# Performance work log

Measured on AMD Instinct MI355X. Metric: run time of the kernel, lower is better.

Reference implementation:

```python
import jax, jax.numpy as jnp
import numpy as np

N_NODES = 10000
N_EDGES = 160000
N_GRAPHS = 100
D = 32
E_DIM = 6
Q = 96
C = 2
EPS = 1e-5
S2S_STEPS = 3


def _bn(x, gamma, beta):
    # BatchNorm1d in training mode: normalize over the batch (row) axis
    mu = jnp.mean(x, axis=0)
    var = jnp.var(x, axis=0)
    return gamma * (x - mu) * jax.lax.rsqrt(var + EPS) + beta


def _mlp_layer(x, w, b, gamma, beta):
    # Linear -> ReLU -> BatchNorm1d (one block of the MLP helper)
    return _bn(jax.nn.relu(x @ w.T + b), gamma, beta)


def _nnconv(x, src, dst, edge_attr, nw, nb, ng, nbeta, root, bias):
    # edge MLP -> per-edge [D, D] weight matrices
    w = _mlp_layer(edge_attr, nw, nb, ng, nbeta).reshape(-1, D, D)  # [E, D, D]
    msg = jnp.einsum('ei,eio->eo', x[src], w)                       # per-edge matvec
    agg = jax.ops.segment_sum(msg, dst, num_segments=N_NODES)      # aggr='add'
    return agg + x @ root + bias                                    # root weight + bias


def _set2set(x, batch, w_ih, w_hh, b_ih, b_hh):
    h = jnp.zeros((N_GRAPHS, Q), x.dtype)
    c = jnp.zeros((N_GRAPHS, Q), x.dtype)
    q_star = jnp.zeros((N_GRAPHS, 2 * Q), x.dtype)
    for _ in range(S2S_STEPS):
        gates = q_star @ w_ih.T + b_ih + h @ w_hh.T + b_hh  # [B, 4Q], gate order i,f,g,o
        i, f, g, o = jnp.split(gates, 4, axis=1)
        c = jax.nn.sigmoid(f) * c + jax.nn.sigmoid(i) * jnp.tanh(g)
        h = jax.nn.sigmoid(o) * jnp.tanh(c)
        e = jnp.sum(x * h[batch], axis=-1)  # [N] attention logits
        emax = jax.ops.segment_max(e, batch, num_segments=N_GRAPHS)
        emax = jnp.where(jnp.isfinite(emax), emax, 0.0)
        a = jnp.exp(e - emax[batch])
        asum = jax.ops.segment_sum(a, batch, num_segments=N_GRAPHS)
        a = a / asum[batch]
        r = jax.ops.segment_sum(a[:, None] * x, batch, num_segments=N_GRAPHS)  # [B, Q]
        q_star = jnp.concatenate([h, r], axis=1)
    return q_star  # [B, 2Q]


def setup_inputs() -> dict:
    key = jax.random.key(0)
    ks = iter(jax.random.split(key, 48))
    def rn(shape, fan_in):
        return jax.random.normal(next(ks), shape, dtype=jnp.float32) * (1.0 / np.sqrt(fan_in))
    d = {}
    d['x'] = jax.random.normal(next(ks), (N_NODES, D), dtype=jnp.float32)
    d['edge_attr'] = jax.random.uniform(next(ks), (N_EDGES, E_DIM), dtype=jnp.float32)
    # conv1 edge-MLP + root + bias
    d['c1_nn_w'] = rn((D * D, E_DIM), E_DIM); d['c1_nn_b'] = jnp.zeros((D * D,), jnp.float32)
    d['c1_nn_g'] = jnp.ones((D * D,), jnp.float32); d['c1_nn_beta'] = jnp.zeros((D * D,), jnp.float32)
    d['c1_root'] = rn((D, D), D); d['c1_bias'] = jnp.zeros((D,), jnp.float32)
    # conv2
    d['c2_nn_w'] = rn((D * D, E_DIM), E_DIM); d['c2_nn_b'] = jnp.zeros((D * D,), jnp.float32)
    d['c2_nn_g'] = jnp.ones((D * D,), jnp.float32); d['c2_nn_beta'] = jnp.zeros((D * D,), jnp.float32)
    d['c2_root'] = rn((D, D), D); d['c2_bias'] = jnp.zeros((D,), jnp.float32)
    # lin1: MLP([2D, Q])
    d['lin1_w'] = rn((Q, 2 * D), 2 * D); d['lin1_b'] = jnp.zeros((Q,), jnp.float32)
    d['lin1_g'] = jnp.ones((Q,), jnp.float32); d['lin1_beta'] = jnp.zeros((Q,), jnp.float32)
    # Set2Set LSTM: input 2Q -> hidden Q
    d['lstm_w_ih'] = rn((4 * Q, 2 * Q), 2 * Q); d['lstm_w_hh'] = rn((4 * Q, Q), Q)
    d['lstm_b_ih'] = jnp.zeros((4 * Q,), jnp.float32); d['lstm_b_hh'] = jnp.zeros((4 * Q,), jnp.float32)
    # S2Slin: Linear(2Q, Q)
    d['s2s_w'] = rn((Q, 2 * Q), 2 * Q); d['s2s_b'] = jnp.zeros((Q,), jnp.float32)
    # mlp1: MLP([Q, Q, C])
    d['m1_w'] = rn((Q, Q), Q); d['m1_b'] = jnp.zeros((Q,), jnp.float32)
    d['m1_g'] = jnp.ones((Q,), jnp.float32); d['m1_beta'] = jnp.zeros((Q,), jnp.float32)
    d['m2_w'] = rn((C, Q), Q); d['m2_b'] = jnp.zeros((C,), jnp.float32)
    d['m2_g'] = jnp.ones((C,), jnp.float32); d['m2_beta'] = jnp.zeros((C,), jnp.float32)
    # graph structure
    d['edge_src'] = jax.random.randint(next(ks), (N_EDGES,), 0, N_NODES, dtype=jnp.int32)
    d['edge_dst'] = jax.random.randint(next(ks), (N_EDGES,), 0, N_NODES, dtype=jnp.int32)
    d['batch'] = jnp.sort(jax.random.randint(next(ks), (N_NODES,), 0, N_GRAPHS, dtype=jnp.int32))
    return d


def reference(x, edge_attr,
              c1_nn_w, c1_nn_b, c1_nn_g, c1_nn_beta, c1_root, c1_bias,
              c2_nn_w, c2_nn_b, c2_nn_g, c2_nn_beta, c2_root, c2_bias,
              lin1_w, lin1_b, lin1_g, lin1_beta,
              lstm_w_ih, lstm_w_hh, lstm_b_ih, lstm_b_hh,
              s2s_w, s2s_b,
              m1_w, m1_b, m1_g, m1_beta,
              m2_w, m2_b, m2_g, m2_beta,
              edge_src, edge_dst, batch):
    x1 = _nnconv(x, edge_src, edge_dst, edge_attr, c1_nn_w, c1_nn_b, c1_nn_g, c1_nn_beta, c1_root, c1_bias)
    x2 = _nnconv(x1, edge_src, edge_dst, edge_attr, c2_nn_w, c2_nn_b, c2_nn_g, c2_nn_beta, c2_root, c2_bias)
    xc = _mlp_layer(jnp.concatenate([x1, x2], axis=1), lin1_w, lin1_b, lin1_g, lin1_beta)  # [N, Q]
    qs = _set2set(xc, batch, lstm_w_ih, lstm_w_hh, lstm_b_ih, lstm_b_hh)                   # [B, 2Q]
    xg = qs @ s2s_w.T + s2s_b                                                               # [B, Q]
    xg = _mlp_layer(xg, m1_w, m1_b, m1_g, m1_beta)
    out = _mlp_layer(xg, m2_w, m2_b, m2_g, m2_beta)                                         # [B, C]
    return out
```

## Files before the change

kernel.cpp:

```cpp
#include <hip/hip_runtime.h>
#include <math.h>

#define NN 10000
#define NE 160000
#define NG 100
#define DD 32
#define QQ 96
#define EPS 1e-5f
#define S2SCAP 128

typedef float f2 __attribute__((ext_vector_type(2)));

__global__ __launch_bounds__(512) void k_stats7(const float* __restrict__ ea,
        const float* __restrict__ w1, const float* __restrict__ b1,
        const float* __restrict__ w2, const float* __restrict__ b2,
        float* __restrict__ stats) {
    const int tid = threadIdx.x;
    const int chunk = blockIdx.x >> 1;
    const int ct = ((blockIdx.x & 1) << 9) | tid;
    const float* wr1 = w1 + ct * 6;
    const float* wr2 = w2 + ct * 6;
    f2 W0 = {wr1[0], wr2[0]}, W1 = {wr1[1], wr2[1]}, W2 = {wr1[2], wr2[2]};
    f2 W3 = {wr1[3], wr2[3]}, W4 = {wr1[4], wr2[4]}, W5 = {wr1[5], wr2[5]};
    f2 Bb = {b1[ct], b2[ct]};
    f2 S = {0.f, 0.f}, SS = {0.f, 0.f};
    const float* base = ea + chunk * 1536;
#pragma unroll 4
    for (int q = 0; q < 128; ++q) {
        float4 q0 = *reinterpret_cast<const float4*>(base + q * 12);
        float4 q1 = *reinterpret_cast<const float4*>(base + q * 12 + 4);
        float4 q2 = *reinterpret_cast<const float4*>(base + q * 12 + 8);
        {
            f2 y = Bb;
            y = q0.x * W0 + y; y = q0.y * W1 + y; y = q0.z * W2 + y;
            y = q0.w * W3 + y; y = q1.x * W4 + y; y = q1.y * W5 + y;
            f2 r = {fmaxf(y.x, 0.f), fmaxf(y.y, 0.f)};
            S = S + r; SS = r * r + SS;
        }
        {
            f2 y = Bb;
            y = q1.z * W0 + y; y = q1.w * W1 + y; y = q2.x * W2 + y;
            y = q2.y * W3 + y; y = q2.z * W4 + y; y = q2.w * W5 + y;
            f2 r = {fmaxf(y.x, 0.f), fmaxf(y.y, 0.f)};
            S = S + r; SS = r * r + SS;
        }
    }
    atomicAdd(&stats[ct], S.x);
    atomicAdd(&stats[1024 + ct], SS.x);
    atomicAdd(&stats[2048 + ct], S.y);
    atomicAdd(&stats[3072 + ct], SS.y);
}

__global__ __launch_bounds__(256) void k_root(const float* __restrict__ x,
        const float* __restrict__ root, const float* __restrict__ bias,
        float* __restrict__ out,
        int doFin, const float* __restrict__ stats,
        const float* __restrict__ g1, const float* __restrict__ beta1,
        const float* __restrict__ g2, const float* __restrict__ beta2,
        const float* __restrict__ nw1, const float* __restrict__ nb1,
        const float* __restrict__ nw2, const float* __restrict__ nb2,
        float* __restrict__ wpack) {
    const int tid = threadIdx.x;
    if (doFin && blockIdx.x == gridDim.x - 1) {
        const float invE = 1.f / NE;
        for (int j = tid; j < 2048; j += 256) {
            int cv = j >> 10, col = j & 1023;
            const float* st = stats + cv * 2048;
            const float* g = cv ? g2 : g1;
            const float* bt = cv ? beta2 : beta1;
            const float* w = (cv ? nw2 : nw1) + col * 6;
            const float* nb = cv ? nb2 : nb1;
            float mean = st[col] * invE;
            float var = fmaxf(st[1024 + col] * invE - mean * mean, 0.f);
            float a = g[col] * rsqrtf(var + EPS);
            float b = bt[col] - mean * a;
            float* rec = wpack + cv * 12288 + col * 12;
            rec[0] = w[0]; rec[1] = w[1]; rec[2] = w[2];
            rec[3] = w[3]; rec[4] = w[4]; rec[5] = w[5];
            rec[6] = nb[col]; rec[7] = a; rec[8] = b;
        }
        return;
    }
    __shared__ float rlds[1024];
#pragma unroll
    for (int r = 0; r < 4; ++r) rlds[tid + 256 * r] = root[tid + 256 * r];
    __syncthreads();
    const int o = tid & 31;
    const int gg = tid >> 5;
    const int n = blockIdx.x * 8 + gg;
    if (n >= NN) return;
    const int half = tid & 32;
    float xs = x[n * 32 + o];
    float acc = bias[o];
#pragma unroll
    for (int i = 0; i < 32; ++i) {
        float xi = __shfl(xs, half | i);
        acc = fmaf(xi, rlds[i * 32 + o], acc);
    }
    out[n * 32 + o] = acc;
}

#define CACCP(PTR, XK, M) { \
    float4 _wa = *reinterpret_cast<const float4*>(PTR); \
    float4 _wb = *reinterpret_cast<const float4*>((PTR) + 4); \
    float _bv = (PTR)[8]; \
    float _y = _wb.z; \
    _y = fmaf(e0, _wa.x, _y); _y = fmaf(e1, _wa.y, _y); _y = fmaf(e2, _wa.z, _y); \
    _y = fmaf(e3, _wa.w, _y); _y = fmaf(e4, _wb.x, _y); _y = fmaf(e5, _wb.y, _y); \
    float _t = fmaf(_wb.w, fmaxf(_y, 0.f), _bv); M = fmaf(XK, _t, M); }

__global__ __launch_bounds__(256) void k_conv(const float* __restrict__ xin,
        const float* __restrict__ ea, const int* __restrict__ src, const int* __restrict__ dst,
        const float* __restrict__ wp, float* __restrict__ agg) {
    __shared__ float part[4][16][32];
    const int tid = threadIdx.x;
    const int lane = tid & 63;
    const int w = tid >> 6;
    const int p = lane >> 5;
    const int o = lane & 31;

    const float* r0 = wp + (((((w << 3) + 0 + p) << 5) | o) * 12);
    const float* r1 = wp + (((((w << 3) + 2 + p) << 5) | o) * 12);
    const float* r2 = wp + (((((w << 3) + 4 + p) << 5) | o) * 12);
    const float* r3 = wp + (((((w << 3) + 6 + p) << 5) | o) * 12);

    const int base0 = blockIdx.x * 80;
#pragma unroll 1
    for (int ch = 0; ch < 5; ++ch) {
        const int base = base0 + ch * 16;
#pragma unroll 4
        for (int m = 0; m < 16; ++m) {
            const int e = base + m;
            const int sc = src[e];
            const float* er = ea + e * 6;
            float e0 = er[0], e1 = er[1], e2 = er[2], e3 = er[3], e4 = er[4], e5 = er[5];
            const float* xr = xin + sc * 32 + (w << 3);
            float4 qa = *reinterpret_cast<const float4*>(xr);
            float4 qb = *reinterpret_cast<const float4*>(xr + 4);
            float xA = p ? qa.y : qa.x, xB = p ? qa.w : qa.z;
            float xC = p ? qb.y : qb.x, xD = p ? qb.w : qb.z;
            float msg = 0.f;
            CACCP(r0, xA, msg) CACCP(r1, xB, msg) CACCP(r2, xC, msg) CACCP(r3, xD, msg)
            msg += __shfl_xor(msg, 32, 64);
            if (p == 0) part[w][m][o] = msg;
        }
        __syncthreads();
        {
            const int m = tid >> 5;
            const int e = base + m;
            const int dd = dst[e];
            float sum = part[0][m][o] + part[1][m][o] + part[2][m][o] + part[3][m][o];
            atomicAdd(&agg[dd * 32 + o], sum);
            const int m2 = m + 8;
            const int e2 = base + m2;
            const int dd2 = dst[e2];
            float sum2 = part[0][m2][o] + part[1][m2][o] + part[2][m2][o] + part[3][m2][o];
            atomicAdd(&agg[dd2 * 32 + o], sum2);
        }
        __syncthreads();
    }
}

__global__ __launch_bounds__(384) void k_lin1a(const float* __restrict__ x1,
        const float* __restrict__ x2, const float* __restrict__ lw, const float* __restrict__ lb,
        float* __restrict__ pre, float* __restrict__ gsum, float* __restrict__ gsumsq) {
    __shared__ float cat[4][64];
    __shared__ float sh_s[96], sh_ss[96];
    const int tid = threadIdx.x;
    const int np = tid / 96;
    const int q = tid - np * 96;
    float w[64];
#pragma unroll
    for (int k = 0; k < 64; ++k) w[k] = lw[q * 64 + k];
    const float bq = lb[q];
    float s = 0.f, ss = 0.f;
    for (int nb = blockIdx.x * 4; nb < NN; nb += gridDim.x * 4) {
        __syncthreads();
        if (tid < 256) {
            int n2 = tid >> 6, k = tid & 63;
            cat[n2][k] = (k < 32) ? x1[(nb + n2) * 32 + k] : x2[(nb + n2) * 32 + (k - 32)];
        }
        __syncthreads();
        float v = bq;
#pragma unroll
        for (int k = 0; k < 64; ++k) v = fmaf(cat[np][k], w[k], v);
        float r = fmaxf(v, 0.f);
        pre[(nb + np) * 96 + q] = r;
        s += r; ss = fmaf(r, r, ss);
    }
    __syncthreads();
    if (tid < 96) { sh_s[tid] = 0.f; sh_ss[tid] = 0.f; }
    __syncthreads();
    atomicAdd(&sh_s[q], s);
    atomicAdd(&sh_ss[q], ss);
    __syncthreads();
    if (tid < 96) {
        atomicAdd(&gsum[tid], sh_s[tid]);
        atomicAdd(&gsumsq[tid], sh_ss[tid]);
    }
}

__global__ __launch_bounds__(512) void k_s2s(const float* __restrict__ pre,
        const int* __restrict__ batch,
        const float* __restrict__ gsum, const float* __restrict__ gsumsq,
        const float* __restrict__ lg, const float* __restrict__ lbeta,
        const float* __restrict__ w_ih, const float* __restrict__ w_hh,
        const float* __restrict__ b_ih, const float* __restrict__ b_hh,
        float* __restrict__ qs_g, float* __restrict__ e_ws) {
    __shared__ float xcs[S2SCAP * 96];
    __shared__ float aws[S2SCAP];
    __shared__ float qs[192], h[96], c[96], gates[384];
    __shared__ float ab_a[96], ab_b[96], hA[96], bh[96];
    __shared__ float redm[8], reds[8];
    __shared__ float racc_s[5][96];
    __shared__ float sh_scal[3];
    __shared__ int sse[2];
    const int tid = threadIdx.x;
    const int wid = tid >> 6, lane = tid & 63;
    const int b = blockIdx.x;
    if (tid < 2) {
        int key = b + tid, lo = 0, hi = NN;
        while (lo < hi) { int mid = (lo + hi) >> 1; if (batch[mid] < key) lo = mid + 1; else hi = mid; }
        sse[tid] = lo;
    }
    if (tid < 192) qs[tid] = 0.f;
    if (tid < 96) {
        h[tid] = 0.f; c[tid] = 0.f;
        const float invN = 1.f / NN;
        float mean = gsum[tid] * invN;
        float var = fmaxf(gsumsq[tid] * invN - mean * mean, 0.f);
        float a = lg[tid] * rsqrtf(var + EPS);
        ab_a[tid] = a;
        ab_b[tid] = lbeta[tid] - mean * a;
    }
    __syncthreads();
    const int s = sse[0], t = sse[1];
    const int cnt = t - s;
    const bool fits = (cnt <= S2SCAP);
    if (fits) {
        for (int idx = tid; idx < cnt * 96; idx += 512) xcs[idx] = pre[s * 96 + idx];
    }
    const float* pb = fits ? (const float*)xcs : (pre + s * 96);
    float* ewp = fits ? (float*)aws : (e_ws + s);
    __syncthreads();
    for (int step = 0; step < 3; ++step) {
        if (tid < 384) {
            float acc = b_ih[tid] + b_hh[tid];
            const float* wi = &w_ih[tid * 192];
#pragma unroll 8
            for (int k = 0; k < 192; ++k) acc = fmaf(qs[k], wi[k], acc);
            const float* wh = &w_hh[tid * 96];
#pragma unroll 8
            for (int k = 0; k < 96; ++k) acc = fmaf(h[k], wh[k], acc);
            gates[tid] = acc;
        }
        __syncthreads();
        if (tid < 96) {
            float ig = 1.f / (1.f + __expf(-gates[tid]));
            float fg = 1.f / (1.f + __expf(-gates[96 + tid]));
            float gg = tanhf(gates[192 + tid]);
            float og = 1.f / (1.f + __expf(-gates[288 + tid]));
            float cn = fg * c[tid] + ig * gg;
            c[tid] = cn;
            float hn = og * tanhf(cn);
            h[tid] = hn;
            hA[tid] = ab_a[tid] * hn;
            bh[tid] = ab_b[tid] * hn;
        }
        __syncthreads();
        if (tid < 64) {
            float v = bh[tid] + (tid < 32 ? bh[64 + tid] : 0.f);
#pragma unroll
            for (int off = 32; off > 0; off >>= 1) v += __shfl_down(v, off);
            if (tid == 0) sh_scal[2] = v;
        }
        __syncthreads();
        const float hb = sh_scal[2];
        float pmax = -INFINITY;
        for (int u = tid; u < cnt; u += 512) {
            const float* xr = pb + u * 96;
            float acc = hb;
#pragma unroll
            for (int k4 = 0; k4 < 24; ++k4) {
                float4 v = *reinterpret_cast<const float4*>(xr + k4 * 4);
                acc = fmaf(v.x, hA[k4 * 4], acc);
                acc = fmaf(v.y, hA[k4 * 4 + 1], acc);
                acc = fmaf(v.z, hA[k4 * 4 + 2], acc);
                acc = fmaf(v.w, hA[k4 * 4 + 3], acc);
            }
            ewp[u] = acc;
            pmax = fmaxf(pmax, acc);
        }
#pragma unroll
        for (int off = 32; off > 0; off >>= 1) pmax = fmaxf(pmax, __shfl_down(pmax, off));
        if (lane == 0) redm[wid] = pmax;
        __syncthreads();
        if (tid == 0) {
            float m = redm[0];
#pragma unroll
            for (int i = 1; i < 8; ++i) m = fmaxf(m, redm[i]);
            if (!isfinite(m)) m = 0.f;
            sh_scal[0] = m;
        }
        __syncthreads();
        const float emax = sh_scal[0];
        float pa = 0.f;
        for (int u = tid; u < cnt; u += 512) {
            float a = __expf(ewp[u] - emax);
            ewp[u] = a;
            pa += a;
        }
#pragma unroll
        for (int off = 32; off > 0; off >>= 1) pa += __shfl_down(pa, off);
        if (lane == 0) reds[wid] = pa;
        __syncthreads();
        if (tid == 0) {
            float a2 = 0.f;
#pragma unroll
            for (int i = 0; i < 8; ++i) a2 += reds[i];
            sh_scal[1] = (a2 > 0.f) ? 1.f / a2 : 0.f;
        }
        __syncthreads();
        const int g = tid / 96, q = tid - g * 96;
        if (tid < 480) {
            float racc = 0.f;
            for (int u = g; u < cnt; u += 5)
                racc = fmaf(ewp[u], pb[u * 96 + q], racc);
            racc_s[g][q] = racc;
        }
        __syncthreads();
        if (tid < 96) {
            float inv = sh_scal[1];
            float racc5 = racc_s[0][tid] + racc_s[1][tid] + racc_s[2][tid]
                        + racc_s[3][tid] + racc_s[4][tid];
            float rq = (inv > 0.f) ? fmaf(ab_a[tid], racc5 * inv, ab_b[tid]) : 0.f;
            qs[tid] = h[tid];
            qs[96 + tid] = rq;
        }
        __syncthreads();
    }
    if (tid < 192) qs_g[b * 192 + tid] = qs[tid];
}

__global__ __launch_bounds__(128) void k_xg(const float* __restrict__ qs_g,
        const float* __restrict__ sw, const float* __restrict__ sb,
        const float* __restrict__ m1w, const float* __restrict__ m1b,
        float* __restrict__ pre, float* __restrict__ gsum, float* __restrict__ gsumsq) {
    __shared__ float xg0[96];
    const int tid = threadIdx.x;
    const int b = blockIdx.x;
    if (tid < 96) {
        const float* q = &qs_g[b * 192];
        float acc = sb[tid];
        const float* w = &sw[tid * 192];
#pragma unroll 8
        for (int k = 0; k < 192; ++k) acc = fmaf(q[k], w[k], acc);
        xg0[tid] = acc;
    }
    __syncthreads();
    if (tid < 96) {
        float acc = m1b[tid];
        const float* w = &m1w[tid * 96];
#pragma unroll 8
        for (int k = 0; k < 96; ++k) acc = fmaf(xg0[k], w[k], acc);
        float r = fmaxf(acc, 0.f);
        pre[b * 96 + tid] = r;
        atomicAdd(&gsum[tid], r);
        atomicAdd(&gsumsq[tid], r * r);
    }
}

__global__ __launch_bounds__(256) void k_tail(const float* __restrict__ pre,
        const float* __restrict__ gsum, const float* __restrict__ gsumsq,
        const float* __restrict__ g1, const float* __restrict__ beta1,
        const float* __restrict__ m2w, const float* __restrict__ m2b,
        const float* __restrict__ g2, const float* __restrict__ beta2,
        float* __restrict__ out) {
    __shared__ float xg1[100][97];
    __shared__ float pre2[200];
    __shared__ float ab2[4];
    const int tid = threadIdx.x;
    if (tid < 96) {
        const float invN = 1.f / NG;
        float mean = gsum[tid] * invN;
        float var = fmaxf(gsumsq[tid] * invN - mean * mean, 0.f);
        float a = g1[tid] * rsqrtf(var + EPS);
        float bb = beta1[tid] - mean * a;
        for (int n = 0; n < NG; ++n)
            xg1[n][tid] = fmaf(a, pre[n * 96 + tid], bb);
    }
    __syncthreads();
    if (tid < 200) {
        int n = tid >> 1, cc = tid & 1;
        float acc = m2b[cc];
        const float* w = &m2w[cc * 96];
#pragma unroll 8
        for (int k = 0; k < 96; ++k) acc = fmaf(xg1[n][k], w[k], acc);
        pre2[tid] = fmaxf(acc, 0.f);
    }
    __syncthreads();
    if (tid < 2) {
        float s = 0.f, ss = 0.f;
        for (int n = 0; n < NG; ++n) { float v = pre2[n * 2 + tid]; s += v; ss = fmaf(v, v, ss); }
        const float invN = 1.f / NG;
        float mean = s * invN;
        float var = fmaxf(ss * invN - mean * mean, 0.f);
        float a = g2[tid] * rsqrtf(var + EPS);
        ab2[tid] = a;
        ab2[2 + tid] = beta2[tid] - mean * a;
    }
    __syncthreads();
    if (tid < 200) {
        int cc = tid & 1;
        out[tid] = fmaf(ab2[cc], pre2[tid], ab2[2 + cc]);
    }
}

extern "C" void kernel_launch(void* const* d_in, const int* in_sizes, int n_in,
                              void* d_out, int out_size, void* d_ws, size_t ws_size,
                              hipStream_t stream) {
    (void)in_sizes; (void)n_in; (void)out_size; (void)ws_size;
    const float* x       = (const float*)d_in[0];
    const float* ea      = (const float*)d_in[1];
    const float* c1w     = (const float*)d_in[2];
    const float* c1b     = (const float*)d_in[3];
    const float* c1g     = (const float*)d_in[4];
    const float* c1beta  = (const float*)d_in[5];
    const float* c1root  = (const float*)d_in[6];
    const float* c1bias  = (const float*)d_in[7];
    const float* c2w     = (const float*)d_in[8];
    const float* c2b     = (const float*)d_in[9];
    const float* c2g     = (const float*)d_in[10];
    const float* c2beta  = (const float*)d_in[11];
    const float* c2root  = (const float*)d_in[12];
    const float* c2bias  = (const float*)d_in[13];
    const float* lin1w   = (const float*)d_in[14];
    const float* lin1b   = (const float*)d_in[15];
    const float* lin1g   = (const float*)d_in[16];
    const float* lin1bt  = (const float*)d_in[17];
    const float* wih     = (const float*)d_in[18];
    const float* whh     = (const float*)d_in[19];
    const float* bih     = (const float*)d_in[20];
    const float* bhh     = (const float*)d_in[21];
    const float* s2sw    = (const float*)d_in[22];
    const float* s2sb    = (const float*)d_in[23];
    const float* m1w     = (const float*)d_in[24];
    const float* m1b     = (const float*)d_in[25];
    const float* m1g     = (const float*)d_in[26];
    const float* m1beta  = (const float*)d_in[27];
    const float* m2w     = (const float*)d_in[28];
    const float* m2b     = (const float*)d_in[29];
    const float* m2g     = (const float*)d_in[30];
    const float* m2beta  = (const float*)d_in[31];
    const int* src       = (const int*)d_in[32];
    const int* dst       = (const int*)d_in[33];
    const int* batch     = (const int*)d_in[34];

    float* ws = (float*)d_ws;
    float* stats  = ws;
    float* linst  = ws + 8192;
    float* m1st   = ws + 8384;
    float* wpack  = ws + 8704;
    float* x1     = wpack + 24576;
    float* x2     = x1 + 320000;
    float* prelin = x2 + 320000;
    float* e_ws   = prelin + 960000;
    float* qs_g   = e_ws + 10000;
    float* prem1  = qs_g + 19200;

    hipMemsetAsync(ws, 0, 8576 * sizeof(float), stream);

    k_stats7<<<1250, 512, 0, stream>>>(ea, c1w, c1b, c2w, c2b, stats);

    k_root<<<1251, 256, 0, stream>>>(x, c1root, c1bias, x1,
                                     1, stats, c1g, c1beta, c2g, c2beta,
                                     c1w, c1b, c2w, c2b, wpack);
    k_conv<<<2000, 256, 0, stream>>>(x, ea, src, dst, wpack, x1);

    k_root<<<1250, 256, 0, stream>>>(x1, c2root, c2bias, x2,
                                     0, stats, c1g, c1beta, c2g, c2beta,
                                     c1w, c1b, c2w, c2b, wpack);
    k_conv<<<2000, 256, 0, stream>>>(x1, ea, src, dst, wpack + 12288, x2);

    k_lin1a<<<500, 384, 0, stream>>>(x1, x2, lin1w, lin1b, prelin, linst, linst + 96);

    k_s2s<<<100, 512, 0, stream>>>(prelin, batch, linst, linst + 96, lin1g, lin1bt,
                                   wih, whh, bih, bhh, qs_g, e_ws);

    k_xg<<<100, 128, 0, stream>>>(qs_g, s2sw, s2sb, m1w, m1b, prem1, m1st, m1st + 96);
    k_tail<<<1, 256, 0, stream>>>(prem1, m1st, m1st + 96, m1g, m1beta,
                                  m2w, m2b, m2g, m2beta, (float*)d_out);
}
```

Before: 278.5 us.

## Transpose LSTM weights for coalesced gate loads and pad set2set shared rows

Adds a small kernel that transposes the LSTM input and hidden weight matrices into workspace, so that in the set2set gate computation adjacent threads read consecutive addresses instead of 192/96-strided rows. It also pads the shared-memory node-feature tile to a row stride of 97 to avoid bank conflicts in the per-node dot product. That dot product now uses scalar loads instead of float4 loads. The cost is one extra kernel launch and extra workspace traffic, and the scalar loads may offset part of the bank-conflict saving.

New measurement: 264.8 us. 1.05x faster.

```diff
diff --git a/kernel.cpp b/kernel.cpp
--- a/kernel.cpp
+++ b/kernel.cpp
@@ -51,6 +51,19 @@
     atomicAdd(&stats[3072 + ct], SS.y);
 }
 
+__global__ __launch_bounds__(512) void k_tw(const float* __restrict__ wih,
+        const float* __restrict__ whh, float* __restrict__ wTih, float* __restrict__ wThh) {
+    const int idx = blockIdx.x * 512 + threadIdx.x;
+    if (idx < 73728) {
+        int k = idx / 384, u = idx - k * 384;
+        wTih[idx] = wih[u * 192 + k];
+    }
+    if (idx < 36864) {
+        int k = idx / 384, u = idx - k * 384;
+        wThh[idx] = whh[u * 96 + k];
+    }
+}
+
 __global__ __launch_bounds__(256) void k_root(const float* __restrict__ x,
         const float* __restrict__ root, const float* __restrict__ bias,
         float* __restrict__ out,
@@ -204,10 +217,10 @@
         const int* __restrict__ batch,
         const float* __restrict__ gsum, const float* __restrict__ gsumsq,
         const float* __restrict__ lg, const float* __restrict__ lbeta,
-        const float* __restrict__ w_ih, const float* __restrict__ w_hh,
+        const float* __restrict__ wTih, const float* __restrict__ wThh,
         const float* __restrict__ b_ih, const float* __restrict__ b_hh,
         float* __restrict__ qs_g, float* __restrict__ e_ws) {
-    __shared__ float xcs[S2SCAP * 96];
+    __shared__ float xcs[S2SCAP * 97];
     __shared__ float aws[S2SCAP];
     __shared__ float qs[192], h[96], c[96], gates[384];
     __shared__ float ab_a[96], ab_b[96], hA[96], bh[96];
@@ -238,20 +251,22 @@
     const int cnt = t - s;
     const bool fits = (cnt <= S2SCAP);
     if (fits) {
-        for (int idx = tid; idx < cnt * 96; idx += 512) xcs[idx] = pre[s * 96 + idx];
-    }
+        for (int idx = tid; idx < cnt * 96; idx += 512) {
+            int u = idx / 96, k = idx - u * 96;
+            xcs[u * 97 + k] = pre[s * 96 + idx];
+        }
+    }
+    const int ldp = fits ? 97 : 96;
     const float* pb = fits ? (const float*)xcs : (pre + s * 96);
     float* ewp = fits ? (float*)aws : (e_ws + s);
     __syncthreads();
     for (int step = 0; step < 3; ++step) {
         if (tid < 384) {
             float acc = b_ih[tid] + b_hh[tid];
-            const float* wi = &w_ih[tid * 192];
 #pragma unroll 8
-            for (int k = 0; k < 192; ++k) acc = fmaf(qs[k], wi[k], acc);
-            const float* wh = &w_hh[tid * 96];
+            for (int k = 0; k < 192; ++k) acc = fmaf(qs[k], wTih[k * 384 + tid], acc);
 #pragma unroll 8
-            for (int k = 0; k < 96; ++k) acc = fmaf(h[k], wh[k], acc);
+            for (int k = 0; k < 96; ++k) acc = fmaf(h[k], wThh[k * 384 + tid], acc);
             gates[tid] = acc;
         }
         __syncthreads();
@@ -278,16 +293,10 @@
         const float hb = sh_scal[2];
         float pmax = -INFINITY;
         for (int u = tid; u < cnt; u += 512) {
-            const float* xr = pb + u * 96;
+            const float* xr = pb + u * ldp;
             float acc = hb;
-#pragma unroll
-            for (int k4 = 0; k4 < 24; ++k4) {
-                float4 v = *reinterpret_cast<const float4*>(xr + k4 * 4);
-                acc = fmaf(v.x, hA[k4 * 4], acc);
-                acc = fmaf(v.y, hA[k4 * 4 + 1], acc);
-                acc = fmaf(v.z, hA[k4 * 4 + 2], acc);
-                acc = fmaf(v.w, hA[k4 * 4 + 3], acc);
-            }
+#pragma unroll 8
+            for (int k = 0; k < 96; ++k) acc = fmaf(xr[k], hA[k], acc);
             ewp[u] = acc;
             pmax = fmaxf(pmax, acc);
         }
@@ -325,7 +334,7 @@
         if (tid < 480) {
             float racc = 0.f;
             for (int u = g; u < cnt; u += 5)
-                racc = fmaf(ewp[u], pb[u * 96 + q], racc);
+                racc = fmaf(ewp[u], pb[u * ldp + q], racc);
             racc_s[g][q] = racc;
         }
         __syncthreads();
@@ -461,7 +470,9 @@
     float* linst  = ws + 8192;
     float* m1st   = ws + 8384;
     float* wpack  = ws + 8704;
-    float* x1     = wpack + 24576;
+    float* wTih   = ws + 33280;
+    float* wThh   = wTih + 73728;
+    float* x1     = wThh + 36864;
     float* x2     = x1 + 320000;
     float* prelin = x2 + 320000;
     float* e_ws   = prelin + 960000;
@@ -470,6 +481,8 @@
 
     hipMemsetAsync(ws, 0, 8576 * sizeof(float), stream);
 
+    k_tw<<<144, 512, 0, stream>>>(wih, whh, wTih, wThh);
+
     k_stats7<<<1250, 512, 0, stream>>>(ea, c1w, c1b, c2w, c2b, stats);
 
     k_root<<<1251, 256, 0, stream>>>(x, c1root, c1bias, x1,
@@ -485,7 +498,7 @@
     k_lin1a<<<500, 384, 0, stream>>>(x1, x2, lin1w, lin1b, prelin, linst, linst + 96);
 
     k_s2s<<<100, 512, 0, stream>>>(prelin, batch, linst, linst + 96, lin1g, lin1bt,
-                                   wih, whh, bih, bhh, qs_g, e_ws);
+                                   wTih, wThh, bih, bhh, qs_g, e_ws);
 
     k_xg<<<100, 128, 0, stream>>>(qs_g, s2sw, s2sb, m1w, m1b, prem1, m1st, m1st + 96);
     k_tail<<<1, 256, 0, stream>>>(prem1, m1st, m1st + 96, m1g, m1beta,
```
